# Performance work log

Hardware: AMD Instinct MI355X
Metric: run time of the kernel (lower is better)

## Reference

```python
import jax, jax.numpy as jnp
import numpy as np

C, N, H, OUT, NIN, NSRC, NB = 16, 8192, 181, 3, 2, 32, 8
OMEGA, SCALE = 30.0, 10.0


def _c(a):
    # view trailing dim-2 float array as complex
    return jax.lax.complex(a[..., 0], a[..., 1])


def setup_inputs() -> dict:
    key = jax.random.key(0)
    ks = jax.random.split(key, 20)
    d = {}
    d["inp"] = jax.random.normal(ks[0], (NSRC, N, NIN), jnp.float32)
    d["indices"] = jax.random.randint(ks[1], (C,), 0, NSRC)
    d["model_idx"] = jax.random.randint(ks[2], (C,), 0, C)
    d["bias_idx"] = jax.random.randint(ks[3], (C,), 0, NB)
    # first layer (real weights, in=2)
    d["W0a"] = 0.05 * jax.random.normal(ks[4], (C, NIN, H), jnp.float32)
    d["b0a"] = 0.01 * jax.random.normal(ks[5], (NB, H), jnp.float32)
    d["W0b"] = 0.05 * jax.random.normal(ks[6], (C, NIN, H), jnp.float32)
    d["b0b"] = 0.01 * jax.random.normal(ks[7], (NB, H), jnp.float32)
    # hidden complex layers stored as float[..., 2] (real, imag)
    k = 8
    for name in ["W1a", "b1a", "W1b", "b1b", "W2a", "b2a", "W2b", "b2b"]:
        if name.startswith("W"):
            d[name] = 0.01 * jax.random.normal(ks[k], (C, H, H, 2), jnp.float32)
        else:
            d[name] = 0.01 * jax.random.normal(ks[k], (NB, H, 2), jnp.float32)
        k += 1
    d["Wf"] = 0.05 * jax.random.normal(ks[16], (C, H, OUT, 2), jnp.float32)
    d["bf"] = 0.01 * jax.random.normal(ks[17], (NB, OUT, 2), jnp.float32)
    return d


def _forward(inp, indices, model_idx, bias_idx, W0a, b0a, W0b, b0b,
             W1a, b1a, W1b, b1b, W2a, b2a, W2b, b2b, Wf, bf):
    x = inp[None, indices]  # [1, C, N, in]
    # first Gabor2D layer: real adaptive linear, complex exp activation
    la = jnp.einsum('bcni,cio->bcno', x, W0a[model_idx]) + b0a[bias_idx][None, :, None, :]
    lb = jnp.einsum('bcni,cio->bcno', x, W0b[model_idx]) + b0b[bias_idx][None, :, None, :]
    # exp(1j*omega*la - |scale*la|^2 - |scale*lb|^2), la/lb real here
    x = jnp.exp(jax.lax.complex(-(SCALE * SCALE) * (la * la + lb * lb), OMEGA * la))
    # hidden Gabor2D layers: complex adaptive linear, fused Gabor chain
    for Wa, ba, Wb, bb in ((W1a, b1a, W1b, b1b), (W2a, b2a, W2b, b2b)):
        la = jnp.einsum('bcni,cio->bcno', x, _c(Wa)[model_idx]) + _c(ba)[bias_idx][None, :, None, :]
        lb = jnp.einsum('bcni,cio->bcno', x, _c(Wb)[model_idx]) + _c(bb)[bias_idx][None, :, None, :]
        # arg = 1j*omega*la - scale^2*(|la|^2 + |lb|^2)
        mag = (SCALE * SCALE) * (la.real ** 2 + la.imag ** 2 + lb.real ** 2 + lb.imag ** 2)
        x = jnp.exp(jax.lax.complex(-OMEGA * la.imag - mag, OMEGA * la.real))
    # outermost complex linear; module returns .real for complex output
    out = jnp.einsum('bcni,cio->bcno', x, _c(Wf)[model_idx]) + _c(bf)[bias_idx][None, :, None, :]
    return out.real


def reference(inp, indices, model_idx, bias_idx, W0a, b0a, W0b, b0b,
              W1a, b1a, W1b, b1b, W2a, b2a, W2b, b2b, Wf, bf):
    return _forward(inp, indices, model_idx, bias_idx, W0a, b0a, W0b, b0b,
                    W1a, b1a, W1b, b1b, W2a, b2a, W2b, b2b, Wf, bf)
```

## Files before the change

### kernel.cpp

```cpp
#include <hip/hip_runtime.h>

typedef _Float16 f16;
typedef _Float16 f16x2 __attribute__((ext_vector_type(2)));
typedef _Float16 f16x8 __attribute__((ext_vector_type(8)));
typedef float f32x4 __attribute__((ext_vector_type(4)));

namespace {

constexpr int kC = 16, kN = 8192, kH = 181, kOut = 3;
constexpr int kMB = 64;
constexpr int kKpad = 384;
constexpr int kNT = 48;
constexpr int kKS = 12;
constexpr int kRowB = 784;
constexpr float kOmega = 30.f, kS2 = 100.f;

constexpr size_t kWLayerStride = (size_t)kNT * kKS * 64 * 8;
constexpr size_t kWfOff = kWLayerStride * kC * 2;
constexpr size_t kWfStride = (size_t)kKS * 64 * 8;
constexpr size_t kW0Off = kWfOff + (size_t)kC * kWfStride;
constexpr size_t kW0Stride = (size_t)kNT * 64 * 8;
constexpr size_t kBiasOff = kW0Off + (size_t)kC * kW0Stride;

__device__ __forceinline__ int xadr(int row, int colb) { return row * kRowB + colb; }

__global__ __launch_bounds__(768) void prep_hidden(
    const int* __restrict__ model_idx, const int* __restrict__ bias_idx,
    const float* __restrict__ W1a, const float* __restrict__ W1b,
    const float* __restrict__ W2a, const float* __restrict__ W2b,
    const float* __restrict__ b1a, const float* __restrict__ b1b,
    const float* __restrict__ b2a, const float* __restrict__ b2b,
    f16* __restrict__ ws)
{
  __shared__ float s[kH][2][4][2];
  const int bid = blockIdx.x;
  const int c  = bid / (2 * kNT);
  const int L  = (bid / kNT) % 2;
  const int nt = bid % kNT;
  const int m  = model_idx[c];
  const float* Wa = (L == 0 ? W1a : W2a) + (size_t)m * kH * kH * 2;
  const float* Wb = (L == 0 ? W1b : W2b) + (size_t)m * kH * kH * 2;
  const int t = threadIdx.x;
  if (t < 2 * kH) {
    const int i = t >> 1, br = t & 1;
    const float* src = (br ? Wb : Wa) + ((size_t)i * kH + nt * 4) * 2;
#pragma unroll
    for (int e = 0; e < 8; ++e) {
      const int osub = e >> 1, reim = e & 1;
      s[i][br][osub][reim] = (nt * 4 + osub < kH) ? src[osub * 2 + reim] : 0.f;
    }
  }
  if (t < 16) {
    const int bix = bias_idx[c];
    const float* pa = (L == 0 ? b1a : b2a) + (size_t)bix * kH * 2;
    const float* pb = (L == 0 ? b1b : b2b) + (size_t)bix * kH * 2;
    const int osub = t >> 2, j = t & 3;
    const int q = nt * 4 + osub;
    float v = 0.f;
    if (q < kH) v = (j < 2) ? pa[q * 2 + j] : pb[q * 2 + (j - 2)];
    float* fb = (float*)(ws + kBiasOff);
    fb[((size_t)(c * 2 + L) * 192 + nt * 4) * 4 + t] = v;
  }
  __syncthreads();
  const int ks = t >> 6, lane = t & 63;
  const int kg = lane >> 4, l15 = lane & 15;
  const int osub = l15 >> 2, comp = l15 & 3, br = comp >> 1;
  const int o = nt * 4 + osub;
  f16x8 v;
#pragma unroll
  for (int j = 0; j < 8; ++j) {
    const int k = ks * 32 + kg * 8 + j;
    float f = 0.f;
    if (k < 2 * kH && o < kH) {
      const int i = k >> 1, kodd = k & 1;
      const int reim = kodd ? (1 - (comp & 1)) : (comp & 1);
      f = s[i][br][osub][reim];
      if (kodd && !(comp & 1)) f = -f;
    }
    v[j] = (f16)f;
  }
  *(f16x8*)&ws[(((size_t)(c * 2 + L) * kNT + nt) * kKS + ks) * 512 + lane * 8] = v;
}

__global__ __launch_bounds__(768) void prep_final(
    const int* __restrict__ model_idx, const float* __restrict__ Wf,
    f16* __restrict__ ws)
{
  const int c = blockIdx.x;
  const int m = model_idx[c];
  const int t = threadIdx.x;
  const int ks = t >> 6, lane = t & 63;
  const int kg = lane >> 4, col = lane & 15;
  f16x8 v;
#pragma unroll
  for (int j = 0; j < 8; ++j) {
    const int k = ks * 32 + kg * 8 + j;
    float f = 0.f;
    if (k < 2 * kH && col < kOut) {
      const int i = k >> 1;
      const float* p = &Wf[(((size_t)m * kH + i) * kOut + col) * 2];
      f = (k & 1) ? -p[1] : p[0];
    }
    v[j] = (f16)f;
  }
  *(f16x8*)&ws[kWfOff + ((size_t)c * kKS + ks) * 512 + lane * 8] = v;
}

__global__ __launch_bounds__(256) void prep_l0(
    const int* __restrict__ model_idx,
    const float* __restrict__ W0a, const float* __restrict__ W0b,
    f16* __restrict__ ws)
{
  const int c = blockIdx.x;
  const int m = model_idx[c];
#pragma unroll 1
  for (int it = 0; it < 12; ++it) {
    const int slot = it * 256 + threadIdx.x;
    const int nt = slot >> 6, lane = slot & 63;
    const int kg = lane >> 4, l15 = lane & 15;
    const int osub = l15 >> 2, comp = l15 & 3;
    const int o = nt * 4 + osub;
    f16x8 v = {};
    if (kg == 0 && o < kH && (comp & 1) == 0) {
#pragma unroll
      for (int k = 0; k < 2; ++k) {
        const float f = (comp == 0) ? W0a[(m * 2 + k) * kH + o]
                                    : W0b[(m * 2 + k) * kH + o];
        v[k] = (f16)f;
      }
    }
    *(f16x8*)&ws[kW0Off + (size_t)c * kW0Stride + (size_t)slot * 8] = v;
  }
}

#define ISSUE2(WIN, J0) { WIN[0] = ap[(J0) * 64]; WIN[1] = ap[(J0 + 1) * 64]; }
#define SLOT2(WIN, KSB)                                                        \
  __builtin_amdgcn_sched_barrier(0);                                           \
  __builtin_amdgcn_s_setprio(1);                                               \
  _Pragma("unroll")                                                            \
  for (int k2 = 0; k2 < 2; ++k2) {                                             \
    acc[0] = __builtin_amdgcn_mfma_f32_16x16x32_f16(WIN[k2], B[0][(KSB) + k2], acc[0], 0, 0, 0); \
    acc[1] = __builtin_amdgcn_mfma_f32_16x16x32_f16(WIN[k2], B[1][(KSB) + k2], acc[1], 0, 0, 0); \
    acc[2] = __builtin_amdgcn_mfma_f32_16x16x32_f16(WIN[k2], B[2][(KSB) + k2], acc[2], 0, 0, 0); \
    acc[3] = __builtin_amdgcn_mfma_f32_16x16x32_f16(WIN[k2], B[3][(KSB) + k2], acc[3], 0, 0, 0); \
  }                                                                            \
  __builtin_amdgcn_s_setprio(0);                                               \
  __builtin_amdgcn_sched_barrier(0);

__device__ __forceinline__ void hidden_gemm(
    char* __restrict__ X, const f16x8* __restrict__ wl,
    const float* __restrict__ bp,
    int w, int lane)
{
  const int kg = lane >> 4, l15 = lane & 15;
  f16x8 B[4][kKS];
#pragma unroll
  for (int pt = 0; pt < 4; ++pt)
#pragma unroll
    for (int ks = 0; ks < kKS; ++ks)
      B[pt][ks] = *(const f16x8*)(X + xadr(l15 + 16 * pt, ks * 64 + kg * 16));
  __syncthreads();

  f16x8 A0[2], A1[2], A2[2];
  {
    const f16x8* ap = wl + (size_t)(w * 12) * (kKS * 64) + lane;
    ISSUE2(A0, 0)
    ISSUE2(A1, 2)
  }

#pragma unroll 1
  for (int mi = 0; mi < 12; ++mi) {
    const int nt = w * 12 + mi;
    const int q = nt * 4 + kg;
    const f16x8* ap = wl + (size_t)nt * (kKS * 64) + lane;
    const f32x4 bv = *(const f32x4*)(bp + (size_t)q * 4);
    f32x4 acc[4] = {};
    ISSUE2(A2, 4)   SLOT2(A0, 0)
    ISSUE2(A0, 6)   SLOT2(A1, 2)
    ISSUE2(A1, 8)   SLOT2(A2, 4)
    ISSUE2(A2, 10)  SLOT2(A0, 6)
    ISSUE2(A0, 12)  SLOT2(A1, 8)
    ISSUE2(A1, 14)  SLOT2(A2, 10)
#pragma unroll
    for (int pt = 0; pt < 4; ++pt) {
      const float v0 = acc[pt][0] + bv[0], v1 = acc[pt][1] + bv[1];
      const float v2 = acc[pt][2] + bv[2], v3 = acc[pt][3] + bv[3];
      const float mag = kS2 * (v0 * v0 + v1 * v1 + v2 * v2 + v3 * v3);
      const float amp = __expf(fmaf(-kOmega, v1, -mag));
      const float ph  = kOmega * v0;
      f16x2 pv = {(f16)(amp * __cosf(ph)), (f16)(amp * __sinf(ph))};
      *(f16x2*)(X + xadr(l15 + 16 * pt, q * 4)) = pv;
    }
  }
}

__global__ __launch_bounds__(256, 2)
void wire_main(
    const float* __restrict__ inp, const int* __restrict__ indices,
    const int* __restrict__ model_idx, const int* __restrict__ bias_idx,
    const float* __restrict__ b0a, const float* __restrict__ b0b,
    const float* __restrict__ bf, const f16* __restrict__ wsW,
    float* __restrict__ out)
{
  __shared__ __align__(16) char X[kMB * kRowB];
  const int d = blockIdx.x;
  const int lg = (d & 7) * 256 + (d >> 3);
  const int c = lg >> 7;
  const int n0 = (lg & 127) * kMB;
  const int src = indices[c], m = model_idx[c], bix = bias_idx[c];
  const int tid = threadIdx.x, w = tid >> 6, lane = tid & 63;
  const int kg = lane >> 4, l15 = lane & 15;

  {
    f16x8 Bx[4];
#pragma unroll
    for (int pt = 0; pt < 4; ++pt) {
      const int row = l15 + 16 * pt;
      const float2 xv = *(const float2*)&inp[((size_t)src * kN + n0 + row) * 2];
      f16x8 b = {};
      if (kg == 0) { b[0] = (f16)xv.x; b[1] = (f16)xv.y; }
      Bx[pt] = b;
    }
    const f16x8* w0p = (const f16x8*)(wsW + kW0Off + (size_t)c * kW0Stride);
    const float* b0av = b0a + (size_t)bix * kH;
    const float* b0bv = b0b + (size_t)bix * kH;

    f16x8 aE, aO, aEn, aOn;
    float brE, crE, brO, crO, brEn, crEn, brOn, crOn;
    {
      const int ntE = w * 12, ntO = ntE + 1;
      aE = w0p[ntE * 64 + lane];
      aO = w0p[ntO * 64 + lane];
      const int qE = ntE * 4 + kg, qO = ntO * 4 + kg;
      brE = (qE < kH) ? b0av[qE] : 0.f;  crE = (qE < kH) ? b0bv[qE] : 0.f;
      brO = (qO < kH) ? b0av[qO] : 0.f;  crO = (qO < kH) ? b0bv[qO] : 0.f;
    }
#pragma unroll 1
    for (int it = 0; it < 6; ++it) {
      const int base = w * 12 + it * 2;
      {
        const int ntE = base + 2, ntO = base + 3;
        aEn = w0p[ntE * 64 + lane];
        aOn = w0p[ntO * 64 + lane];
        const int qE = ntE * 4 + kg, qO = ntO * 4 + kg;
        brEn = (qE < kH) ? b0av[qE] : 0.f;  crEn = (qE < kH) ? b0bv[qE] : 0.f;
        brOn = (qO < kH) ? b0av[qO] : 0.f;  crOn = (qO < kH) ? b0bv[qO] : 0.f;
      }
      __builtin_amdgcn_sched_barrier(0);
#pragma unroll
      for (int par = 0; par < 2; ++par) {
        const f16x8 a = par ? aO : aE;
        const float br_ = par ? brO : brE, cr_ = par ? crO : crE;
        const int q = (base + par) * 4 + kg;
        f32x4 acc[4] = {};
        __builtin_amdgcn_s_setprio(1);
        acc[0] = __builtin_amdgcn_mfma_f32_16x16x32_f16(a, Bx[0], acc[0], 0, 0, 0);
        acc[1] = __builtin_amdgcn_mfma_f32_16x16x32_f16(a, Bx[1], acc[1], 0, 0, 0);
        acc[2] = __builtin_amdgcn_mfma_f32_16x16x32_f16(a, Bx[2], acc[2], 0, 0, 0);
        acc[3] = __builtin_amdgcn_mfma_f32_16x16x32_f16(a, Bx[3], acc[3], 0, 0, 0);
        __builtin_amdgcn_s_setprio(0);
#pragma unroll
        for (int pt = 0; pt < 4; ++pt) {
          const float v0 = acc[pt][0] + br_;
          const float v2 = acc[pt][2] + cr_;
          const float mag = kS2 * (v0 * v0 + v2 * v2);
          const float amp = __expf(-mag);
          const float ph  = kOmega * v0;
          f16x2 pv = {(f16)(amp * __cosf(ph)), (f16)(amp * __sinf(ph))};
          *(f16x2*)(&X[0] + xadr(l15 + 16 * pt, q * 4)) = pv;
        }
      }
      __builtin_amdgcn_sched_barrier(0);
      aE = aEn; aO = aOn;
      brE = brEn; crE = crEn; brO = brOn; crO = crOn;
    }
  }
  __syncthreads();
  const float* biasB = (const float*)(wsW + kBiasOff);
  hidden_gemm(X, (const f16x8*)(wsW + (size_t)(c * 2 + 0) * kWLayerStride),
              biasB + (size_t)(c * 2 + 0) * 192 * 4, w, lane);
  __syncthreads();
  hidden_gemm(X, (const f16x8*)(wsW + (size_t)(c * 2 + 1) * kWLayerStride),
              biasB + (size_t)(c * 2 + 1) * 192 * 4, w, lane);
  __syncthreads();
  {
    const f16x8* wf = (const f16x8*)(wsW + kWfOff + (size_t)c * kWfStride);
    f16x8 wfr[kKS];
#pragma unroll
    for (int ks = 0; ks < kKS; ++ks) wfr[ks] = wf[(size_t)ks * 64 + lane];
    __builtin_amdgcn_sched_barrier(0);
    f32x4 facc = {0.f, 0.f, 0.f, 0.f};
#pragma unroll
    for (int ks = 0; ks < kKS; ++ks) {
      f16x8 a = *(const f16x8*)(&X[0] + xadr(l15 + 16 * w, ks * 64 + kg * 16));
      facc = __builtin_amdgcn_mfma_f32_16x16x32_f16(a, wfr[ks], facc, 0, 0, 0);
    }
    if (l15 < kOut) {
      const float bfr = bf[(bix * kOut + l15) * 2];
#pragma unroll
      for (int j = 0; j < 4; ++j) {
        const int row = w * 16 + kg * 4 + j;
        out[((size_t)c * kN + n0 + row) * kOut + l15] = facc[j] + bfr;
      }
    }
  }
}

}

extern "C" void kernel_launch(void* const* d_in, const int* in_sizes, int n_in,
                              void* d_out, int out_size, void* d_ws, size_t ws_size,
                              hipStream_t stream) {
  const float* inp       = (const float*)d_in[0];
  const int*   indices   = (const int*)  d_in[1];
  const int*   model_idx = (const int*)  d_in[2];
  const int*   bias_idx  = (const int*)  d_in[3];
  const float* W0a = (const float*)d_in[4];
  const float* b0a = (const float*)d_in[5];
  const float* W0b = (const float*)d_in[6];
  const float* b0b = (const float*)d_in[7];
  const float* W1a = (const float*)d_in[8];
  const float* b1a = (const float*)d_in[9];
  const float* W1b = (const float*)d_in[10];
  const float* b1b = (const float*)d_in[11];
  const float* W2a = (const float*)d_in[12];
  const float* b2a = (const float*)d_in[13];
  const float* W2b = (const float*)d_in[14];
  const float* b2b = (const float*)d_in[15];
  const float* Wf  = (const float*)d_in[16];
  const float* bff = (const float*)d_in[17];
  f16*   ws  = (f16*)d_ws;
  float* out = (float*)d_out;

  prep_hidden<<<dim3(kC * 2 * kNT), dim3(768), 0, stream>>>(
      model_idx, bias_idx, W1a, W1b, W2a, W2b, b1a, b1b, b2a, b2b, ws);
  prep_final<<<dim3(kC), dim3(768), 0, stream>>>(model_idx, Wf, ws);
  prep_l0<<<dim3(kC), dim3(256), 0, stream>>>(model_idx, W0a, W0b, ws);
  wire_main<<<dim3(kC * (kN / kMB)), dim3(256), 0, stream>>>(
      inp, indices, model_idx, bias_idx, b0a, b0b,
      bff, ws, out);
}
```

Before: 182.3 us.

## Switch hidden-layer GEMMs from 16x16x32 to 32x32x16 MFMA tiles

```diff
diff --git a/kernel.cpp b/kernel.cpp
--- a/kernel.cpp
+++ b/kernel.cpp
@@ -4,6 +4,7 @@
 typedef _Float16 f16x2 __attribute__((ext_vector_type(2)));
 typedef _Float16 f16x8 __attribute__((ext_vector_type(8)));
 typedef float f32x4 __attribute__((ext_vector_type(4)));
+typedef float f32x16 __attribute__((ext_vector_type(16)));
 
 namespace {
 
@@ -12,10 +13,12 @@
 constexpr int kKpad = 384;
 constexpr int kNT = 48;
 constexpr int kKS = 12;
+constexpr int kMT = 24;
+constexpr int kKS2 = 24;
 constexpr int kRowB = 784;
 constexpr float kOmega = 30.f, kS2 = 100.f;
 
-constexpr size_t kWLayerStride = (size_t)kNT * kKS * 64 * 8;
+constexpr size_t kWLayerStride = (size_t)kMT * kKS2 * 64 * 8;
 constexpr size_t kWfOff = kWLayerStride * kC * 2;
 constexpr size_t kWfStride = (size_t)kKS * 64 * 8;
 constexpr size_t kW0Off = kWfOff + (size_t)kC * kWfStride;
@@ -32,54 +35,59 @@
     const float* __restrict__ b2a, const float* __restrict__ b2b,
     f16* __restrict__ ws)
 {
-  __shared__ float s[kH][2][4][2];
+  __shared__ float s[kH][2][8][2];
   const int bid = blockIdx.x;
-  const int c  = bid / (2 * kNT);
-  const int L  = (bid / kNT) % 2;
-  const int nt = bid % kNT;
+  const int c  = bid / (2 * kMT);
+  const int L  = (bid / kMT) % 2;
+  const int mt = bid % kMT;
   const int m  = model_idx[c];
   const float* Wa = (L == 0 ? W1a : W2a) + (size_t)m * kH * kH * 2;
   const float* Wb = (L == 0 ? W1b : W2b) + (size_t)m * kH * kH * 2;
   const int t = threadIdx.x;
   if (t < 2 * kH) {
     const int i = t >> 1, br = t & 1;
-    const float* src = (br ? Wb : Wa) + ((size_t)i * kH + nt * 4) * 2;
-#pragma unroll
-    for (int e = 0; e < 8; ++e) {
+    const float* base = (br ? Wb : Wa) + (size_t)i * kH * 2;
+#pragma unroll
+    for (int e = 0; e < 16; ++e) {
       const int osub = e >> 1, reim = e & 1;
-      s[i][br][osub][reim] = (nt * 4 + osub < kH) ? src[osub * 2 + reim] : 0.f;
-    }
-  }
-  if (t < 16) {
+      const int o = mt * 8 + osub;
+      s[i][br][osub][reim] = (o < kH) ? base[o * 2 + reim] : 0.f;
+    }
+  }
+  if (t < 32) {
     const int bix = bias_idx[c];
     const float* pa = (L == 0 ? b1a : b2a) + (size_t)bix * kH * 2;
     const float* pb = (L == 0 ? b1b : b2b) + (size_t)bix * kH * 2;
     const int osub = t >> 2, j = t & 3;
-    const int q = nt * 4 + osub;
+    const int q = mt * 8 + osub;
     float v = 0.f;
     if (q < kH) v = (j < 2) ? pa[q * 2 + j] : pb[q * 2 + (j - 2)];
     float* fb = (float*)(ws + kBiasOff);
-    fb[((size_t)(c * 2 + L) * 192 + nt * 4) * 4 + t] = v;
-  }
-  __syncthreads();
-  const int ks = t >> 6, lane = t & 63;
-  const int kg = lane >> 4, l15 = lane & 15;
-  const int osub = l15 >> 2, comp = l15 & 3, br = comp >> 1;
-  const int o = nt * 4 + osub;
-  f16x8 v;
-#pragma unroll
-  for (int j = 0; j < 8; ++j) {
-    const int k = ks * 32 + kg * 8 + j;
-    float f = 0.f;
-    if (k < 2 * kH && o < kH) {
-      const int i = k >> 1, kodd = k & 1;
-      const int reim = kodd ? (1 - (comp & 1)) : (comp & 1);
-      f = s[i][br][osub][reim];
-      if (kodd && !(comp & 1)) f = -f;
-    }
-    v[j] = (f16)f;
-  }
-  *(f16x8*)&ws[(((size_t)(c * 2 + L) * kNT + nt) * kKS + ks) * 512 + lane * 8] = v;
+    fb[((size_t)(c * 2 + L) * 192 + mt * 8) * 4 + t] = v;
+  }
+  __syncthreads();
+  const int lane = t & 63;
+  const int l31 = lane & 31, hi = lane >> 5;
+  const int osub = l31 >> 2, comp = l31 & 3, br = comp >> 1;
+  const int o = mt * 8 + osub;
+#pragma unroll 1
+  for (int pass = 0; pass < 2; ++pass) {
+    const int ks = pass * 12 + (t >> 6);
+    f16x8 v;
+#pragma unroll
+    for (int j = 0; j < 8; ++j) {
+      const int k = ks * 16 + hi * 8 + j;
+      float f = 0.f;
+      if (k < 2 * kH && o < kH) {
+        const int i = k >> 1, kodd = k & 1;
+        const int reim = kodd ? (1 - (comp & 1)) : (comp & 1);
+        f = s[i][br][osub][reim];
+        if (kodd && !(comp & 1)) f = -f;
+      }
+      v[j] = (f16)f;
+    }
+    *(f16x8*)&ws[(((size_t)(c * 2 + L) * kMT + mt) * kKS2 + ks) * 512 + lane * 8] = v;
+  }
 }
 
 __global__ __launch_bounds__(768) void prep_final(
@@ -134,15 +142,13 @@
 }
 
 #define ISSUE2(WIN, J0) { WIN[0] = ap[(J0) * 64]; WIN[1] = ap[(J0 + 1) * 64]; }
-#define SLOT2(WIN, KSB)                                                        \
+#define SLOT32(WIN, KSB)                                                       \
   __builtin_amdgcn_sched_barrier(0);                                           \
   __builtin_amdgcn_s_setprio(1);                                               \
   _Pragma("unroll")                                                            \
   for (int k2 = 0; k2 < 2; ++k2) {                                             \
-    acc[0] = __builtin_amdgcn_mfma_f32_16x16x32_f16(WIN[k2], B[0][(KSB) + k2], acc[0], 0, 0, 0); \
-    acc[1] = __builtin_amdgcn_mfma_f32_16x16x32_f16(WIN[k2], B[1][(KSB) + k2], acc[1], 0, 0, 0); \
-    acc[2] = __builtin_amdgcn_mfma_f32_16x16x32_f16(WIN[k2], B[2][(KSB) + k2], acc[2], 0, 0, 0); \
-    acc[3] = __builtin_amdgcn_mfma_f32_16x16x32_f16(WIN[k2], B[3][(KSB) + k2], acc[3], 0, 0, 0); \
+    acc0 = __builtin_amdgcn_mfma_f32_32x32x16_f16(WIN[k2], B[0][(KSB) + k2], acc0, 0, 0, 0); \
+    acc1 = __builtin_amdgcn_mfma_f32_32x32x16_f16(WIN[k2], B[1][(KSB) + k2], acc1, 0, 0, 0); \
   }                                                                            \
   __builtin_amdgcn_s_setprio(0);                                               \
   __builtin_amdgcn_sched_barrier(0);
@@ -152,45 +158,59 @@
     const float* __restrict__ bp,
     int w, int lane)
 {
-  const int kg = lane >> 4, l15 = lane & 15;
-  f16x8 B[4][kKS];
-#pragma unroll
-  for (int pt = 0; pt < 4; ++pt)
-#pragma unroll
-    for (int ks = 0; ks < kKS; ++ks)
-      B[pt][ks] = *(const f16x8*)(X + xadr(l15 + 16 * pt, ks * 64 + kg * 16));
+  const int l31 = lane & 31, hi = lane >> 5;
+  f16x8 B[2][kKS2];
+#pragma unroll
+  for (int pt = 0; pt < 2; ++pt)
+#pragma unroll
+    for (int ks = 0; ks < kKS2; ++ks)
+      B[pt][ks] = *(const f16x8*)(X + xadr(l31 + 32 * pt, ks * 32 + hi * 16));
   __syncthreads();
 
   f16x8 A0[2], A1[2], A2[2];
   {
-    const f16x8* ap = wl + (size_t)(w * 12) * (kKS * 64) + lane;
+    const f16x8* ap = wl + (size_t)(w * 6) * (kKS2 * 64) + lane;
     ISSUE2(A0, 0)
     ISSUE2(A1, 2)
   }
 
 #pragma unroll 1
-  for (int mi = 0; mi < 12; ++mi) {
-    const int nt = w * 12 + mi;
-    const int q = nt * 4 + kg;
-    const f16x8* ap = wl + (size_t)nt * (kKS * 64) + lane;
-    const f32x4 bv = *(const f32x4*)(bp + (size_t)q * 4);
-    f32x4 acc[4] = {};
-    ISSUE2(A2, 4)   SLOT2(A0, 0)
-    ISSUE2(A0, 6)   SLOT2(A1, 2)
-    ISSUE2(A1, 8)   SLOT2(A2, 4)
-    ISSUE2(A2, 10)  SLOT2(A0, 6)
-    ISSUE2(A0, 12)  SLOT2(A1, 8)
-    ISSUE2(A1, 14)  SLOT2(A2, 10)
-#pragma unroll
-    for (int pt = 0; pt < 4; ++pt) {
-      const float v0 = acc[pt][0] + bv[0], v1 = acc[pt][1] + bv[1];
-      const float v2 = acc[pt][2] + bv[2], v3 = acc[pt][3] + bv[3];
-      const float mag = kS2 * (v0 * v0 + v1 * v1 + v2 * v2 + v3 * v3);
-      const float amp = __expf(fmaf(-kOmega, v1, -mag));
-      const float ph  = kOmega * v0;
-      f16x2 pv = {(f16)(amp * __cosf(ph)), (f16)(amp * __sinf(ph))};
-      *(f16x2*)(X + xadr(l15 + 16 * pt, q * 4)) = pv;
-    }
+  for (int mi = 0; mi < 6; ++mi) {
+    const int mt = w * 6 + mi;
+    const f16x8* ap = wl + (size_t)mt * (kKS2 * 64) + lane;
+    f32x4 bv0 = *(const f32x4*)(bp + (size_t)(mt * 8 + 0 + hi) * 4);
+    f32x4 bv1 = *(const f32x4*)(bp + (size_t)(mt * 8 + 2 + hi) * 4);
+    f32x4 bv2 = *(const f32x4*)(bp + (size_t)(mt * 8 + 4 + hi) * 4);
+    f32x4 bv3 = *(const f32x4*)(bp + (size_t)(mt * 8 + 6 + hi) * 4);
+    f32x16 acc0 = {}, acc1 = {};
+    ISSUE2(A2, 4)   SLOT32(A0, 0)
+    ISSUE2(A0, 6)   SLOT32(A1, 2)
+    ISSUE2(A1, 8)   SLOT32(A2, 4)
+    ISSUE2(A2, 10)  SLOT32(A0, 6)
+    ISSUE2(A0, 12)  SLOT32(A1, 8)
+    ISSUE2(A1, 14)  SLOT32(A2, 10)
+    ISSUE2(A2, 16)  SLOT32(A0, 12)
+    ISSUE2(A0, 18)  SLOT32(A1, 14)
+    ISSUE2(A1, 20)  SLOT32(A2, 16)
+    ISSUE2(A2, 22)  SLOT32(A0, 18)
+    ISSUE2(A0, 24)  SLOT32(A1, 20)
+    ISSUE2(A1, 26)  SLOT32(A2, 22)
+#pragma unroll
+    for (int pt = 0; pt < 2; ++pt)
+#pragma unroll
+      for (int g = 0; g < 4; ++g) {
+        const f32x4 bq = (g == 0) ? bv0 : (g == 1) ? bv1 : (g == 2) ? bv2 : bv3;
+        const float v0 = (pt ? acc1 : acc0)[4 * g + 0] + bq[0];
+        const float v1 = (pt ? acc1 : acc0)[4 * g + 1] + bq[1];
+        const float v2 = (pt ? acc1 : acc0)[4 * g + 2] + bq[2];
+        const float v3 = (pt ? acc1 : acc0)[4 * g + 3] + bq[3];
+        const float mag = kS2 * (v0 * v0 + v1 * v1 + v2 * v2 + v3 * v3);
+        const float amp = __expf(fmaf(-kOmega, v1, -mag));
+        const float ph  = kOmega * v0;
+        f16x2 pv = {(f16)(amp * __cosf(ph)), (f16)(amp * __sinf(ph))};
+        const int n = mt * 8 + g * 2 + hi;
+        *(f16x2*)(X + xadr(l31 + 32 * pt, n * 4)) = pv;
+      }
   }
 }
 
@@ -332,7 +352,7 @@
   f16*   ws  = (f16*)d_ws;
   float* out = (float*)d_out;
 
-  prep_hidden<<<dim3(kC * 2 * kNT), dim3(768), 0, stream>>>(
+  prep_hidden<<<dim3(kC * 2 * kMT), dim3(768), 0, stream>>>(
       model_idx, bias_idx, W1a, W1b, W2a, W2b, b1a, b1b, b2a, b2b, ws);
   prep_final<<<dim3(kC), dim3(768), 0, stream>>>(model_idx, Wf, ws);
   prep_l0<<<dim3(kC), dim3(256), 0, stream>>>(model_idx, W0a, W0b, ws);
```

After: 242.5 us. 1.33x slower.
